# Optimization experiments

Measured on AMD Instinct MI355X. Metric: run time of the kernel, lower is better.

## Reference

```python
import jax, jax.numpy as jnp
import numpy as np

NUM_QUBITS = 10
NUM_LAYERS = 5
OBS = 10          # observation_size == num_qubits (required by input_scaling indexing)
NUM_OUTPUTS = 4   # num_actions, discretize=False
BATCH = 4096


def _bcast(theta, n):
    # theta: scalar or (B,) -> broadcastable against (B, 2, 2, ..., 2)
    return jnp.reshape(jnp.asarray(theta), (-1,) + (1,) * n)


def _ry(st, theta, q, n):
    # st: (B,) + (2,)*n complex64; per-sample RY(theta) on qubit q
    t = _bcast(theta, n) * 0.5
    c, s = jnp.cos(t), jnp.sin(t)
    s0 = jax.lax.index_in_dim(st, 0, axis=q + 1, keepdims=True)
    s1 = jax.lax.index_in_dim(st, 1, axis=q + 1, keepdims=True)
    return jnp.concatenate([c * s0 - s * s1, s * s0 + c * s1], axis=q + 1)


def _rz(st, theta, q, n):
    t = _bcast(theta, n) * 0.5
    s0 = jax.lax.index_in_dim(st, 0, axis=q + 1, keepdims=True)
    s1 = jax.lax.index_in_dim(st, 1, axis=q + 1, keepdims=True)
    return jnp.concatenate([jnp.exp(-1j * t) * s0, jnp.exp(1j * t) * s1], axis=q + 1)


def _cnot(st, c, t):
    # flip target axis on the control=1 slab; pure index ops (no residuals in bwd)
    s0 = jax.lax.index_in_dim(st, 0, axis=c + 1, keepdims=True)
    s1 = jax.lax.index_in_dim(st, 1, axis=c + 1, keepdims=True)
    s1 = jnp.flip(s1, axis=t + 1)
    return jnp.concatenate([s0, s1], axis=c + 1)


def _layer(st, x, isc, w, n, obs):
    # isc: (2n,) input_scaling row, w: (2n,) weights row
    for i in range(obs):
        st = _ry(st, isc[i] * x[:, i], i, n)
        st = _rz(st, isc[i + obs] * x[:, i], i, n)
    for i in range(n):
        st = _rz(st, w[i], i, n)
    for i in range(n):
        st = _ry(st, w[i + n], i, n)
    if n == 2:
        st = _cnot(st, 0, 1)
    else:
        for i in range(n):
            st = _cnot(st, i, (i + 1) % n)
    return st


_layer_ckpt = jax.checkpoint(_layer, static_argnums=(4, 5))


def _circuit(x, input_scaling, weights, n, num_layers, obs, num_outputs):
    B = x.shape[0]
    st = jnp.zeros((B,) + (2,) * n, dtype=jnp.complex64)
    st = st.at[(slice(None),) + (0,) * n].set(1.0)  # |0...0>
    for layer in range(num_layers):
        st = _layer_ckpt(st, x, input_scaling[layer], weights[layer], n, obs)
    probs = jnp.real(st * jnp.conj(st))
    outs = []
    for i in range(num_outputs):
        axes = tuple(a for a in range(1, n + 1) if a != i + 1)
        pi = jnp.sum(probs, axis=axes)  # (B, 2)
        outs.append(pi[:, 0] - pi[:, 1])  # <Z_i>
    return jnp.stack(outs, axis=1)


def setup_inputs() -> dict:
    key = jax.random.key(0)
    k1, k2 = jax.random.split(key)
    x = jax.random.normal(k1, (BATCH, OBS), dtype=jnp.float32)
    input_scaling = jnp.ones((NUM_LAYERS, 2 * NUM_QUBITS), dtype=jnp.float32)
    weights = jax.random.uniform(k2, (NUM_LAYERS, 2 * NUM_QUBITS), minval=-np.pi, maxval=np.pi, dtype=jnp.float32)
    output_scaling = jnp.ones((NUM_OUTPUTS,), dtype=jnp.float32)
    return {"x": x, "input_scaling": input_scaling, "weights": weights, "output_scaling": output_scaling}


def reference(x, input_scaling, weights, output_scaling):
    z = _circuit(x, input_scaling, weights, NUM_QUBITS, NUM_LAYERS, OBS, NUM_OUTPUTS)
    return z * output_scaling  # (B, num_actions); discretize=False -> actions = scaled expvals
```

## Files before the change

### kernel.cpp

```cpp
#include <hip/hip_runtime.h>
#include <hip/hip_fp16.h>


constexpr int NQ  = 10;
constexpr int NL  = 5;
constexpr int OBS = 10;

typedef float f2 __attribute__((ext_vector_type(2)));

__device__ __forceinline__ float readlane_f(float v, int l) {
    return __int_as_float(__builtin_amdgcn_readlane(__float_as_int(v), l));
}
__device__ __forceinline__ int h2i(__half2 v) { int i; __builtin_memcpy(&i, &v, 4); return i; }
__device__ __forceinline__ __half2 i2h(int i) { __half2 v; __builtin_memcpy(&v, &i, 4); return v; }

__device__ __forceinline__ __half2 bperm_h2(int byte_addr, __half2 v) {
    return i2h(__builtin_amdgcn_ds_bpermute(byte_addr, h2i(v)));
}
template <int CTRL>
__device__ __forceinline__ __half2 dpp_h2(__half2 v) {
    return i2h(__builtin_amdgcn_update_dpp(0, h2i(v), CTRL, 0xF, 0xF, true));
}
__device__ __forceinline__ __half2 xor_lane(__half2 v, int M, int a16, int a32) {
    switch (M) {
    case 1:  return dpp_h2<0xB1>(v);
    case 2:  return dpp_h2<0x4E>(v);
    case 8:  return dpp_h2<0x128>(v);
    case 4:  return dpp_h2<0x141>(dpp_h2<0x1B>(v));
    case 16: return bperm_h2(a16, v);
    default: return bperm_h2(a32, v);
    }
}
__device__ __forceinline__ __half2 swap_h2(__half2 v) { return __lowhigh2highlow(v); }
__device__ __forceinline__ __half2 acc4(__half2 a, __half2 b, __half2 c, __half2 d,
                                        __half2 e, __half2 f, __half2 g, __half2 h) {
    return __hfma2(a, b, __hfma2(c, d, __hfma2(e, f, __hmul2(g, h))));
}

__global__ __launch_bounds__(256, 4) void qsim_kernel(
    const float* __restrict__ x,
    const float* __restrict__ isc,
    const float* __restrict__ w,
    const float* __restrict__ oscale,
    float* __restrict__ out,
    int B)
{
    const int lane = threadIdx.x & 63;
    const int wid  = (blockIdx.x * blockDim.x + threadIdx.x) >> 6;
    if (wid >= B) return;

    float cUR, cUI, cVR, cVI;
    {
        const int g   = (lane < 50) ? lane : 49;
        const int q   = g % 10;
        const int lyr = g / 10;
        const float xq    = x[wid * OBS + q];
        const float alpha = isc[lyr * 2 * NQ + q]      * xq;
        const float beta  = isc[lyr * 2 * NQ + NQ + q] * xq;
        const float gamma = w[lyr * 2 * NQ + q];
        const float delta = w[lyr * 2 * NQ + NQ + q];
        float sa, ca, sp, cp, sd, cd;
        __sincosf(0.5f * alpha,          &sa, &ca);
        __sincosf(0.5f * (beta + gamma), &sp, &cp);
        __sincosf(0.5f * delta,          &sd, &cd);
        const float A = cd * ca, Bt = sd * sa;
        const float C = cd * sa, D  = sd * ca;
        cUR = (A - Bt) * cp;
        cUI = -(A + Bt) * sp;
        cVR = (C + D) * cp;
        cVI = (C - D) * sp;
    }

    const int a16 = (lane ^ 16) * 4;
    const int a32 = (lane ^ 32) * 4;
    const int cnot_src  = (lane ^ (lane >> 1));
    const int addr_even = cnot_src * 4;
    const int addr_odd  = (cnot_src ^ 32) * 4;

    __half2 c[16];

    {
        float Lr = 1.f, Li = 0.f;
#pragma unroll
        for (int q = 4; q < 10; ++q) {
            const float ur = readlane_f(cUR, q), ui = readlane_f(cUI, q);
            const float vr = readlane_f(cVR, q), vi = readlane_f(cVI, q);
            const int M = 1 << (9 - q);
            const float fr = (lane & M) ? vr : ur;
            const float fi = (lane & M) ? vi : ui;
            const float nr = Lr * fr - Li * fi;
            const float ni = Lr * fi + Li * fr;
            Lr = nr; Li = ni;
        }
        f2 cf[16];
        cf[0] = (f2){Lr, Li};
#pragma unroll
        for (int r = 1; r < 16; ++r) cf[r] = (f2){0.f, 0.f};
#pragma unroll
        for (int q = 3; q >= 0; --q) {
            const int m = 1 << (3 - q);
            const float ur = readlane_f(cUR, q), ui = readlane_f(cUI, q);
            const float vr = readlane_f(cVR, q), vi = readlane_f(cVI, q);
#pragma unroll
            for (int r0 = 0; r0 < 16; ++r0) {
                if (r0 >= m) continue;
                const f2 s = cf[r0];
                cf[r0 | m] = (f2){ s.x*vr - s.y*vi, s.x*vi + s.y*vr };
                cf[r0]     = (f2){ s.x*ur - s.y*ui, s.x*ui + s.y*ur };
            }
        }
#pragma unroll
        for (int r = 0; r < 16; ++r) c[r] = __floats2half2_rn(cf[r].x, cf[r].y);
    }

#define SWAPR(i, j) { __half2 _t = c[i]; c[i] = c[j]; c[j] = _t; }

    for (int layer = 0; layer < NL; ++layer) {
        const int base = layer * NQ;

        if (layer > 0) {
#pragma unroll
            for (int q = 0; q < NQ; ++q) {
                const float ur = readlane_f(cUR, base + q);
                const float ui = readlane_f(cUI, base + q);
                const float vr = readlane_f(cVR, base + q);
                const float vi = readlane_f(cVI, base + q);

                if (q < 4) {
                    const __half2 kUU  = __floats2half2_rn(ur, ur);
                    const __half2 kUIm = __floats2half2_rn(-ui, ui);
                    const __half2 kVVn = __floats2half2_rn(-vr, -vr);
                    const __half2 kVV  = __floats2half2_rn(vr, vr);
                    const __half2 kVIm = __floats2half2_rn(-vi, vi);
                    const __half2 kUIp = __floats2half2_rn(ui, -ui);
                    const int m = 1 << (3 - q);
#pragma unroll
                    for (int r0 = 0; r0 < 16; ++r0) {
                        if (r0 & m) continue;
                        const int r1 = r0 | m;
                        const __half2 c0 = c[r0], c1 = c[r1];
                        const __half2 c0s = swap_h2(c0), c1s = swap_h2(c1);
                        c[r0] = acc4(kUU, c0, kUIm, c0s, kVVn, c1, kVIm, c1s);
                        c[r1] = acc4(kVV, c0, kVIm, c0s, kUU,  c1, kUIp, c1s);
                    }
                } else {
                    const int  M   = 1 << (9 - q);
                    const bool bit = (lane & M) != 0;
                    const float Pi = bit ? -ui : ui;
                    const float Qr = bit ?  vr : -vr;
                    const __half2 kUUb = __floats2half2_rn(ur, ur);
                    const __half2 kPI  = __floats2half2_rn(-Pi, Pi);
                    const __half2 kQR  = __floats2half2_rn(Qr, Qr);
                    const __half2 kVIb = __floats2half2_rn(-vi, vi);
#pragma unroll
                    for (int r = 0; r < 16; ++r) {
                        const __half2 mv = c[r];
                        const __half2 pv = xor_lane(mv, M, a16, a32);
                        c[r] = acc4(kUUb, mv, kPI, swap_h2(mv), kQR, pv, kVIb, swap_h2(pv));
                    }
                }
            }
        }

        if (layer < NL - 1) {
            SWAPR(8, 12) SWAPR(9, 13) SWAPR(10, 14) SWAPR(11, 15)
            SWAPR(4, 6)  SWAPR(5, 7)  SWAPR(12, 14) SWAPR(13, 15)
            SWAPR(2, 3)  SWAPR(6, 7)  SWAPR(10, 11) SWAPR(14, 15)
#pragma unroll
            for (int r = 0; r < 16; ++r) {
                const int addr = (r & 1) ? addr_odd : addr_even;
                c[r] = bperm_h2(addr, c[r]);
            }
            const bool ctl = (lane & 1) != 0;
#pragma unroll
            for (int r = 0; r < 8; ++r) {
                const __half2 t0 = c[r], t1 = c[r + 8];
                c[r]     = ctl ? t1 : t0;
                c[r + 8] = ctl ? t0 : t1;
            }
        }
    }

    const float sL = (__popc(lane) & 1) ? -1.f : 1.f;
    float z0 = 0.f, z1 = 0.f, z2 = 0.f, z3 = 0.f;
#pragma unroll
    for (int r = 0; r < 16; ++r) {
        const float cr = __low2float(c[r]), ci = __high2float(c[r]);
        const float pv  = cr * cr + ci * ci;
        const float pvl = sL * pv;
        z0 += (__popc(r & 7)  & 1) ? -pvl : pvl;
        z1 += (__popc(r & 12) & 1) ? -pv  : pv;
        z2 += (__popc(r & 14) & 1) ? -pv  : pv;
        z3 += (__popc(r & 15) & 1) ? -pv  : pv;
    }
    {
        auto dpp_f32 = [](float v, int ctrl) -> float {
            switch (ctrl) {
            case 0xB1:  return __int_as_float(__builtin_amdgcn_update_dpp(0, __float_as_int(v), 0xB1, 0xF, 0xF, true));
            case 0x4E:  return __int_as_float(__builtin_amdgcn_update_dpp(0, __float_as_int(v), 0x4E, 0xF, 0xF, true));
            case 0x128: return __int_as_float(__builtin_amdgcn_update_dpp(0, __float_as_int(v), 0x128, 0xF, 0xF, true));
            default:    return __int_as_float(__builtin_amdgcn_update_dpp(0,
                               __builtin_amdgcn_update_dpp(0, __float_as_int(v), 0x1B, 0xF, 0xF, true),
                               0x141, 0xF, 0xF, true));
            }
        };
        z0 += dpp_f32(z0, 0xB1);  z1 += dpp_f32(z1, 0xB1);
        z2 += dpp_f32(z2, 0xB1);  z3 += dpp_f32(z3, 0xB1);
        z0 += dpp_f32(z0, 0x4E);  z1 += dpp_f32(z1, 0x4E);
        z2 += dpp_f32(z2, 0x4E);  z3 += dpp_f32(z3, 0x4E);
        z0 += dpp_f32(z0, 0);     z1 += dpp_f32(z1, 0);
        z2 += dpp_f32(z2, 0);     z3 += dpp_f32(z3, 0);
        z0 += dpp_f32(z0, 0x128); z1 += dpp_f32(z1, 0x128);
        z2 += dpp_f32(z2, 0x128); z3 += dpp_f32(z3, 0x128);
        z0 += __int_as_float(__builtin_amdgcn_ds_bpermute(a16, __float_as_int(z0)));
        z1 += __int_as_float(__builtin_amdgcn_ds_bpermute(a16, __float_as_int(z1)));
        z2 += __int_as_float(__builtin_amdgcn_ds_bpermute(a16, __float_as_int(z2)));
        z3 += __int_as_float(__builtin_amdgcn_ds_bpermute(a16, __float_as_int(z3)));
        z0 += __int_as_float(__builtin_amdgcn_ds_bpermute(a32, __float_as_int(z0)));
        z1 += __int_as_float(__builtin_amdgcn_ds_bpermute(a32, __float_as_int(z1)));
        z2 += __int_as_float(__builtin_amdgcn_ds_bpermute(a32, __float_as_int(z2)));
        z3 += __int_as_float(__builtin_amdgcn_ds_bpermute(a32, __float_as_int(z3)));
    }
    if (lane == 0) {
        out[wid * 4 + 0] = z0 * oscale[0];
        out[wid * 4 + 1] = z1 * oscale[1];
        out[wid * 4 + 2] = z2 * oscale[2];
        out[wid * 4 + 3] = z3 * oscale[3];
    }
#undef SWAPR
}

extern "C" void kernel_launch(void* const* d_in, const int* in_sizes, int n_in,
                              void* d_out, int out_size, void* d_ws, size_t ws_size,
                              hipStream_t stream) {
    const float* x      = (const float*)d_in[0];
    const float* isc    = (const float*)d_in[1];
    const float* w      = (const float*)d_in[2];
    const float* oscale = (const float*)d_in[3];
    float* out = (float*)d_out;

    const int B = in_sizes[0] / OBS;
    const int threads = 256;
    const int blocks = (B * 64 + threads - 1) / threads;
    qsim_kernel<<<blocks, threads, 0, stream>>>(x, isc, w, oscale, out, B);
}
```

Measured before the change: 89.27 us.

## Process two batch samples per wavefront to interleave independent state updates

Each wavefront now simulates two batch samples at once, keeping two register-resident half-precision state vectors and interleaving their gate updates, lane permutes and reductions. This gives more independent instructions to hide DPP/bpermute and FMA latency and halves the wave count, with launch bounds lowered to allow the higher register use. The cost is more register pressure and lower occupancy. An odd batch size would drop the last sample.

```diff
diff --git a/kernel.cpp b/kernel.cpp
--- a/kernel.cpp
+++ b/kernel.cpp
@@ -31,44 +31,102 @@
     default: return bperm_h2(a32, v);
     }
 }
+__device__ __forceinline__ int xor_lane_i(int v, int M, int a16, int a32) {
+    switch (M) {
+    case 1:  return __builtin_amdgcn_update_dpp(0, v, 0xB1, 0xF, 0xF, true);
+    case 2:  return __builtin_amdgcn_update_dpp(0, v, 0x4E, 0xF, 0xF, true);
+    case 8:  return __builtin_amdgcn_update_dpp(0, v, 0x128, 0xF, 0xF, true);
+    case 4:  return __builtin_amdgcn_update_dpp(0,
+                 __builtin_amdgcn_update_dpp(0, v, 0x1B, 0xF, 0xF, true),
+                 0x141, 0xF, 0xF, true);
+    case 16: return __builtin_amdgcn_ds_bpermute(a16, v);
+    default: return __builtin_amdgcn_ds_bpermute(a32, v);
+    }
+}
 __device__ __forceinline__ __half2 swap_h2(__half2 v) { return __lowhigh2highlow(v); }
 __device__ __forceinline__ __half2 acc4(__half2 a, __half2 b, __half2 c, __half2 d,
                                         __half2 e, __half2 f, __half2 g, __half2 h) {
     return __hfma2(a, b, __hfma2(c, d, __hfma2(e, f, __hmul2(g, h))));
 }
 
-__global__ __launch_bounds__(256, 4) void qsim_kernel(
+__device__ __forceinline__ void gate_coeffs(const float* __restrict__ xrow,
+                                            const float* __restrict__ isc,
+                                            const float* __restrict__ w,
+                                            int lyr, int q,
+                                            float& UR, float& UI, float& VR, float& VI) {
+    const float xq    = xrow[q];
+    const float alpha = isc[lyr * 2 * NQ + q]      * xq;
+    const float beta  = isc[lyr * 2 * NQ + NQ + q] * xq;
+    const float gamma = w[lyr * 2 * NQ + q];
+    const float delta = w[lyr * 2 * NQ + NQ + q];
+    float sa, ca, sp, cp, sd, cd;
+    __sincosf(0.5f * alpha,          &sa, &ca);
+    __sincosf(0.5f * (beta + gamma), &sp, &cp);
+    __sincosf(0.5f * delta,          &sd, &cd);
+    const float A = cd * ca, Bt = sd * sa;
+    const float C = cd * sa, D  = sd * ca;
+    UR = (A - Bt) * cp;
+    UI = -(A + Bt) * sp;
+    VR = (C + D) * cp;
+    VI = (C - D) * sp;
+}
+
+__device__ __forceinline__ void build_state(__half2* c, int lane,
+                                            float cUR, float cUI,
+                                            float cVR, float cVI) {
+    float Lr = 1.f, Li = 0.f;
+#pragma unroll
+    for (int q = 4; q < 10; ++q) {
+        const float ur = readlane_f(cUR, q), ui = readlane_f(cUI, q);
+        const float vr = readlane_f(cVR, q), vi = readlane_f(cVI, q);
+        const int M = 1 << (9 - q);
+        const float fr = (lane & M) ? vr : ur;
+        const float fi = (lane & M) ? vi : ui;
+        const float nr = Lr * fr - Li * fi;
+        const float ni = Lr * fi + Li * fr;
+        Lr = nr; Li = ni;
+    }
+    f2 cf[16];
+    cf[0] = (f2){Lr, Li};
+#pragma unroll
+    for (int r = 1; r < 16; ++r) cf[r] = (f2){0.f, 0.f};
+#pragma unroll
+    for (int q = 3; q >= 0; --q) {
+        const int m = 1 << (3 - q);
+        const float ur = readlane_f(cUR, q), ui = readlane_f(cUI, q);
+        const float vr = readlane_f(cVR, q), vi = readlane_f(cVI, q);
+#pragma unroll
+        for (int r0 = 0; r0 < 16; ++r0) {
+            if (r0 >= m) continue;
+            const f2 s = cf[r0];
+            cf[r0 | m] = (f2){ s.x*vr - s.y*vi, s.x*vi + s.y*vr };
+            cf[r0]     = (f2){ s.x*ur - s.y*ui, s.x*ui + s.y*ur };
+        }
+    }
+#pragma unroll
+    for (int r = 0; r < 16; ++r) c[r] = __floats2half2_rn(cf[r].x, cf[r].y);
+}
+
+__global__ __launch_bounds__(256, 2) void qsim_kernel(
     const float* __restrict__ x,
     const float* __restrict__ isc,
     const float* __restrict__ w,
     const float* __restrict__ oscale,
     float* __restrict__ out,
-    int B)
+    int halfB)
 {
     const int lane = threadIdx.x & 63;
-    const int wid  = (blockIdx.x * blockDim.x + threadIdx.x) >> 6;
-    if (wid >= B) return;
-
-    float cUR, cUI, cVR, cVI;
+    const int wv   = (blockIdx.x * blockDim.x + threadIdx.x) >> 6;
+    if (wv >= halfB) return;
+    const int widA = 2 * wv, widB = 2 * wv + 1;
+
+    float aUR, aUI, aVR, aVI, bUR, bUI, bVR, bVI;
     {
         const int g   = (lane < 50) ? lane : 49;
         const int q   = g % 10;
         const int lyr = g / 10;
-        const float xq    = x[wid * OBS + q];
-        const float alpha = isc[lyr * 2 * NQ + q]      * xq;
-        const float beta  = isc[lyr * 2 * NQ + NQ + q] * xq;
-        const float gamma = w[lyr * 2 * NQ + q];
-        const float delta = w[lyr * 2 * NQ + NQ + q];
-        float sa, ca, sp, cp, sd, cd;
-        __sincosf(0.5f * alpha,          &sa, &ca);
-        __sincosf(0.5f * (beta + gamma), &sp, &cp);
-        __sincosf(0.5f * delta,          &sd, &cd);
-        const float A = cd * ca, Bt = sd * sa;
-        const float C = cd * sa, D  = sd * ca;
-        cUR = (A - Bt) * cp;
-        cUI = -(A + Bt) * sp;
-        cVR = (C + D) * cp;
-        cVI = (C - D) * sp;
+        gate_coeffs(x + widA * OBS, isc, w, lyr, q, aUR, aUI, aVR, aVI);
+        gate_coeffs(x + widB * OBS, isc, w, lyr, q, bUR, bUI, bVR, bVI);
     }
 
     const int a16 = (lane ^ 16) * 4;
@@ -77,43 +135,11 @@
     const int addr_even = cnot_src * 4;
     const int addr_odd  = (cnot_src ^ 32) * 4;
 
-    __half2 c[16];
-
-    {
-        float Lr = 1.f, Li = 0.f;
-#pragma unroll
-        for (int q = 4; q < 10; ++q) {
-            const float ur = readlane_f(cUR, q), ui = readlane_f(cUI, q);
-            const float vr = readlane_f(cVR, q), vi = readlane_f(cVI, q);
-            const int M = 1 << (9 - q);
-            const float fr = (lane & M) ? vr : ur;
-            const float fi = (lane & M) ? vi : ui;
-            const float nr = Lr * fr - Li * fi;
-            const float ni = Lr * fi + Li * fr;
-            Lr = nr; Li = ni;
-        }
-        f2 cf[16];
-        cf[0] = (f2){Lr, Li};
-#pragma unroll
-        for (int r = 1; r < 16; ++r) cf[r] = (f2){0.f, 0.f};
-#pragma unroll
-        for (int q = 3; q >= 0; --q) {
-            const int m = 1 << (3 - q);
-            const float ur = readlane_f(cUR, q), ui = readlane_f(cUI, q);
-            const float vr = readlane_f(cVR, q), vi = readlane_f(cVI, q);
-#pragma unroll
-            for (int r0 = 0; r0 < 16; ++r0) {
-                if (r0 >= m) continue;
-                const f2 s = cf[r0];
-                cf[r0 | m] = (f2){ s.x*vr - s.y*vi, s.x*vi + s.y*vr };
-                cf[r0]     = (f2){ s.x*ur - s.y*ui, s.x*ui + s.y*ur };
-            }
-        }
-#pragma unroll
-        for (int r = 0; r < 16; ++r) c[r] = __floats2half2_rn(cf[r].x, cf[r].y);
-    }
-
-#define SWAPR(i, j) { __half2 _t = c[i]; c[i] = c[j]; c[j] = _t; }
+    __half2 cA[16], cB[16];
+    build_state(cA, lane, aUR, aUI, aVR, aVI);
+    build_state(cB, lane, bUR, bUI, bVR, bVI);
+
+#define SWAPR(arr, i, j) { __half2 _t = arr[i]; arr[i] = arr[j]; arr[j] = _t; }
 
     for (int layer = 0; layer < NL; ++layer) {
         const int base = layer * NQ;
@@ -121,111 +147,135 @@
         if (layer > 0) {
 #pragma unroll
             for (int q = 0; q < NQ; ++q) {
-                const float ur = readlane_f(cUR, base + q);
-                const float ui = readlane_f(cUI, base + q);
-                const float vr = readlane_f(cVR, base + q);
-                const float vi = readlane_f(cVI, base + q);
+                const float Aur = readlane_f(aUR, base + q);
+                const float Aui = readlane_f(aUI, base + q);
+                const float Avr = readlane_f(aVR, base + q);
+                const float Avi = readlane_f(aVI, base + q);
+                const float Bur = readlane_f(bUR, base + q);
+                const float Bui = readlane_f(bUI, base + q);
+                const float Bvr = readlane_f(bVR, base + q);
+                const float Bvi = readlane_f(bVI, base + q);
 
                 if (q < 4) {
-                    const __half2 kUU  = __floats2half2_rn(ur, ur);
-                    const __half2 kUIm = __floats2half2_rn(-ui, ui);
-                    const __half2 kVVn = __floats2half2_rn(-vr, -vr);
-                    const __half2 kVV  = __floats2half2_rn(vr, vr);
-                    const __half2 kVIm = __floats2half2_rn(-vi, vi);
-                    const __half2 kUIp = __floats2half2_rn(ui, -ui);
+                    const __half2 AkUU  = __floats2half2_rn(Aur, Aur);
+                    const __half2 AkUIm = __floats2half2_rn(-Aui, Aui);
+                    const __half2 AkVVn = __floats2half2_rn(-Avr, -Avr);
+                    const __half2 AkVV  = __floats2half2_rn(Avr, Avr);
+                    const __half2 AkVIm = __floats2half2_rn(-Avi, Avi);
+                    const __half2 AkUIp = __floats2half2_rn(Aui, -Aui);
+                    const __half2 BkUU  = __floats2half2_rn(Bur, Bur);
+                    const __half2 BkUIm = __floats2half2_rn(-Bui, Bui);
+                    const __half2 BkVVn = __floats2half2_rn(-Bvr, -Bvr);
+                    const __half2 BkVV  = __floats2half2_rn(Bvr, Bvr);
+                    const __half2 BkVIm = __floats2half2_rn(-Bvi, Bvi);
+                    const __half2 BkUIp = __floats2half2_rn(Bui, -Bui);
                     const int m = 1 << (3 - q);
 #pragma unroll
                     for (int r0 = 0; r0 < 16; ++r0) {
                         if (r0 & m) continue;
                         const int r1 = r0 | m;
-                        const __half2 c0 = c[r0], c1 = c[r1];
-                        const __half2 c0s = swap_h2(c0), c1s = swap_h2(c1);
-                        c[r0] = acc4(kUU, c0, kUIm, c0s, kVVn, c1, kVIm, c1s);
-                        c[r1] = acc4(kVV, c0, kVIm, c0s, kUU,  c1, kUIp, c1s);
+                        const __half2 a0 = cA[r0], a1 = cA[r1];
+                        const __half2 b0 = cB[r0], b1 = cB[r1];
+                        const __half2 a0s = swap_h2(a0), a1s = swap_h2(a1);
+                        const __half2 b0s = swap_h2(b0), b1s = swap_h2(b1);
+                        cA[r0] = acc4(AkUU, a0, AkUIm, a0s, AkVVn, a1, AkVIm, a1s);
+                        cB[r0] = acc4(BkUU, b0, BkUIm, b0s, BkVVn, b1, BkVIm, b1s);
+                        cA[r1] = acc4(AkVV, a0, AkVIm, a0s, AkUU,  a1, AkUIp, a1s);
+                        cB[r1] = acc4(BkVV, b0, BkVIm, b0s, BkUU,  b1, BkUIp, b1s);
                     }
                 } else {
                     const int  M   = 1 << (9 - q);
                     const bool bit = (lane & M) != 0;
-                    const float Pi = bit ? -ui : ui;
-                    const float Qr = bit ?  vr : -vr;
-                    const __half2 kUUb = __floats2half2_rn(ur, ur);
-                    const __half2 kPI  = __floats2half2_rn(-Pi, Pi);
-                    const __half2 kQR  = __floats2half2_rn(Qr, Qr);
-                    const __half2 kVIb = __floats2half2_rn(-vi, vi);
+                    const float APi = bit ? -Aui : Aui;
+                    const float AQr = bit ?  Avr : -Avr;
+                    const float BPi = bit ? -Bui : Bui;
+                    const float BQr = bit ?  Bvr : -Bvr;
+                    const __half2 AkUU = __floats2half2_rn(Aur, Aur);
+                    const __half2 AkPI = __floats2half2_rn(-APi, APi);
+                    const __half2 AkQR = __floats2half2_rn(AQr, AQr);
+                    const __half2 AkVI = __floats2half2_rn(-Avi, Avi);
+                    const __half2 BkUU = __floats2half2_rn(Bur, Bur);
+                    const __half2 BkPI = __floats2half2_rn(-BPi, BPi);
+                    const __half2 BkQR = __floats2half2_rn(BQr, BQr);
+                    const __half2 BkVI = __floats2half2_rn(-Bvi, Bvi);
 #pragma unroll
                     for (int r = 0; r < 16; ++r) {
-                        const __half2 mv = c[r];
-                        const __half2 pv = xor_lane(mv, M, a16, a32);
-                        c[r] = acc4(kUUb, mv, kPI, swap_h2(mv), kQR, pv, kVIb, swap_h2(pv));
+                        const __half2 mvA = cA[r];
+                        const __half2 mvB = cB[r];
+                        const __half2 pvA = xor_lane(mvA, M, a16, a32);
+                        const __half2 pvB = xor_lane(mvB, M, a16, a32);
+                        cA[r] = acc4(AkUU, mvA, AkPI, swap_h2(mvA), AkQR, pvA, AkVI, swap_h2(pvA));
+                        cB[r] = acc4(BkUU, mvB, BkPI, swap_h2(mvB), BkQR, pvB, BkVI, swap_h2(pvB));
                     }
                 }
             }
         }
 
         if (layer < NL - 1) {
-            SWAPR(8, 12) SWAPR(9, 13) SWAPR(10, 14) SWAPR(11, 15)
-            SWAPR(4, 6)  SWAPR(5, 7)  SWAPR(12, 14) SWAPR(13, 15)
-            SWAPR(2, 3)  SWAPR(6, 7)  SWAPR(10, 11) SWAPR(14, 15)
+            SWAPR(cA, 8, 12) SWAPR(cA, 9, 13) SWAPR(cA, 10, 14) SWAPR(cA, 11, 15)
+            SWAPR(cB, 8, 12) SWAPR(cB, 9, 13) SWAPR(cB, 10, 14) SWAPR(cB, 11, 15)
+            SWAPR(cA, 4, 6)  SWAPR(cA, 5, 7)  SWAPR(cA, 12, 14) SWAPR(cA, 13, 15)
+            SWAPR(cB, 4, 6)  SWAPR(cB, 5, 7)  SWAPR(cB, 12, 14) SWAPR(cB, 13, 15)
+            SWAPR(cA, 2, 3)  SWAPR(cA, 6, 7)  SWAPR(cA, 10, 11) SWAPR(cA, 14, 15)
+            SWAPR(cB, 2, 3)  SWAPR(cB, 6, 7)  SWAPR(cB, 10, 11) SWAPR(cB, 14, 15)
 #pragma unroll
             for (int r = 0; r < 16; ++r) {
                 const int addr = (r & 1) ? addr_odd : addr_even;
-                c[r] = bperm_h2(addr, c[r]);
+                cA[r] = bperm_h2(addr, cA[r]);
+                cB[r] = bperm_h2(addr, cB[r]);
             }
             const bool ctl = (lane & 1) != 0;
 #pragma unroll
             for (int r = 0; r < 8; ++r) {
-                const __half2 t0 = c[r], t1 = c[r + 8];
-                c[r]     = ctl ? t1 : t0;
-                c[r + 8] = ctl ? t0 : t1;
+                const __half2 tA0 = cA[r], tA1 = cA[r + 8];
+                cA[r]     = ctl ? tA1 : tA0;
+                cA[r + 8] = ctl ? tA0 : tA1;
+                const __half2 tB0 = cB[r], tB1 = cB[r + 8];
+                cB[r]     = ctl ? tB1 : tB0;
+                cB[r + 8] = ctl ? tB0 : tB1;
             }
         }
     }
 
     const float sL = (__popc(lane) & 1) ? -1.f : 1.f;
-    float z0 = 0.f, z1 = 0.f, z2 = 0.f, z3 = 0.f;
+    float zA0 = 0.f, zA1 = 0.f, zA2 = 0.f, zA3 = 0.f;
+    float zB0 = 0.f, zB1 = 0.f, zB2 = 0.f, zB3 = 0.f;
 #pragma unroll
     for (int r = 0; r < 16; ++r) {
-        const float cr = __low2float(c[r]), ci = __high2float(c[r]);
-        const float pv  = cr * cr + ci * ci;
-        const float pvl = sL * pv;
-        z0 += (__popc(r & 7)  & 1) ? -pvl : pvl;
-        z1 += (__popc(r & 12) & 1) ? -pv  : pv;
-        z2 += (__popc(r & 14) & 1) ? -pv  : pv;
-        z3 += (__popc(r & 15) & 1) ? -pv  : pv;
-    }
-    {
-        auto dpp_f32 = [](float v, int ctrl) -> float {
-            switch (ctrl) {
-            case 0xB1:  return __int_as_float(__builtin_amdgcn_update_dpp(0, __float_as_int(v), 0xB1, 0xF, 0xF, true));
-            case 0x4E:  return __int_as_float(__builtin_amdgcn_update_dpp(0, __float_as_int(v), 0x4E, 0xF, 0xF, true));
-            case 0x128: return __int_as_float(__builtin_amdgcn_update_dpp(0, __float_as_int(v), 0x128, 0xF, 0xF, true));
-            default:    return __int_as_float(__builtin_amdgcn_update_dpp(0,
-                               __builtin_amdgcn_update_dpp(0, __float_as_int(v), 0x1B, 0xF, 0xF, true),
-                               0x141, 0xF, 0xF, true));
-            }
-        };
-        z0 += dpp_f32(z0, 0xB1);  z1 += dpp_f32(z1, 0xB1);
-        z2 += dpp_f32(z2, 0xB1);  z3 += dpp_f32(z3, 0xB1);
-        z0 += dpp_f32(z0, 0x4E);  z1 += dpp_f32(z1, 0x4E);
-        z2 += dpp_f32(z2, 0x4E);  z3 += dpp_f32(z3, 0x4E);
-        z0 += dpp_f32(z0, 0);     z1 += dpp_f32(z1, 0);
-        z2 += dpp_f32(z2, 0);     z3 += dpp_f32(z3, 0);
-        z0 += dpp_f32(z0, 0x128); z1 += dpp_f32(z1, 0x128);
-        z2 += dpp_f32(z2, 0x128); z3 += dpp_f32(z3, 0x128);
-        z0 += __int_as_float(__builtin_amdgcn_ds_bpermute(a16, __float_as_int(z0)));
-        z1 += __int_as_float(__builtin_amdgcn_ds_bpermute(a16, __float_as_int(z1)));
-        z2 += __int_as_float(__builtin_amdgcn_ds_bpermute(a16, __float_as_int(z2)));
-        z3 += __int_as_float(__builtin_amdgcn_ds_bpermute(a16, __float_as_int(z3)));
-        z0 += __int_as_float(__builtin_amdgcn_ds_bpermute(a32, __float_as_int(z0)));
-        z1 += __int_as_float(__builtin_amdgcn_ds_bpermute(a32, __float_as_int(z1)));
-        z2 += __int_as_float(__builtin_amdgcn_ds_bpermute(a32, __float_as_int(z2)));
-        z3 += __int_as_float(__builtin_amdgcn_ds_bpermute(a32, __float_as_int(z3)));
+        const float ar = __low2float(cA[r]), ai = __high2float(cA[r]);
+        const float br = __low2float(cB[r]), bi = __high2float(cB[r]);
+        const float pA = ar * ar + ai * ai;
+        const float pB = br * br + bi * bi;
+        const float pAl = sL * pA, pBl = sL * pB;
+        const bool n0 = __popc(r & 7)  & 1;
+        const bool n1 = __popc(r & 12) & 1;
+        const bool n2 = __popc(r & 14) & 1;
+        const bool n3 = __popc(r & 15) & 1;
+        zA0 += n0 ? -pAl : pAl;  zB0 += n0 ? -pBl : pBl;
+        zA1 += n1 ? -pA  : pA;   zB1 += n1 ? -pB  : pB;
+        zA2 += n2 ? -pA  : pA;   zB2 += n2 ? -pB  : pB;
+        zA3 += n3 ? -pA  : pA;   zB3 += n3 ? -pB  : pB;
+    }
+#pragma unroll
+    for (int m = 1; m < 64; m <<= 1) {
+        zA0 += __int_as_float(xor_lane_i(__float_as_int(zA0), m, a16, a32));
+        zB0 += __int_as_float(xor_lane_i(__float_as_int(zB0), m, a16, a32));
+        zA1 += __int_as_float(xor_lane_i(__float_as_int(zA1), m, a16, a32));
+        zB1 += __int_as_float(xor_lane_i(__float_as_int(zB1), m, a16, a32));
+        zA2 += __int_as_float(xor_lane_i(__float_as_int(zA2), m, a16, a32));
+        zB2 += __int_as_float(xor_lane_i(__float_as_int(zB2), m, a16, a32));
+        zA3 += __int_as_float(xor_lane_i(__float_as_int(zA3), m, a16, a32));
+        zB3 += __int_as_float(xor_lane_i(__float_as_int(zB3), m, a16, a32));
     }
     if (lane == 0) {
-        out[wid * 4 + 0] = z0 * oscale[0];
-        out[wid * 4 + 1] = z1 * oscale[1];
-        out[wid * 4 + 2] = z2 * oscale[2];
-        out[wid * 4 + 3] = z3 * oscale[3];
+        out[widA * 4 + 0] = zA0 * oscale[0];
+        out[widA * 4 + 1] = zA1 * oscale[1];
+        out[widA * 4 + 2] = zA2 * oscale[2];
+        out[widA * 4 + 3] = zA3 * oscale[3];
+        out[widB * 4 + 0] = zB0 * oscale[0];
+        out[widB * 4 + 1] = zB1 * oscale[1];
+        out[widB * 4 + 2] = zB2 * oscale[2];
+        out[widB * 4 + 3] = zB3 * oscale[3];
     }
 #undef SWAPR
 }
@@ -239,8 +289,9 @@
     const float* oscale = (const float*)d_in[3];
     float* out = (float*)d_out;
 
-    const int B = in_sizes[0] / OBS;
+    const int B     = in_sizes[0] / OBS;
+    const int halfB = B / 2;
     const int threads = 256;
-    const int blocks = (B * 64 + threads - 1) / threads;
-    qsim_kernel<<<blocks, threads, 0, stream>>>(x, isc, w, oscale, out, B);
-}
+    const int blocks = (halfB * 64 + threads - 1) / threads;
+    qsim_kernel<<<blocks, threads, 0, stream>>>(x, isc, w, oscale, out, halfB);
+}
```

Result: slower. 92.05 us (+3.1%).
